# Kernel tuning notes

Hardware: AMD Instinct MI355X
Metric: run time of the kernel (lower is better)

The kernel has to match this reference:

```python
import jax, jax.numpy as jnp
import numpy as np

D_IN = 1024
D_OUT = 1024
NUM_HEADS = 16
HEAD_DIM = D_OUT // NUM_HEADS


def setup_inputs() -> dict:
    key = jax.random.key(0)
    k_x, k_q, k_k, k_v, k_o, k_ob = jax.random.split(key, 6)
    s_in = 1.0 / np.sqrt(D_IN)
    s_out = 1.0 / np.sqrt(D_OUT)
    return {
        "x": jax.random.normal(k_x, (4, 2048, D_IN), dtype=jnp.float32),
        "W_Q": jax.random.uniform(k_q, (D_IN, D_OUT), jnp.float32, -s_in, s_in),
        "W_K": jax.random.uniform(k_k, (D_IN, D_OUT), jnp.float32, -s_in, s_in),
        "W_V": jax.random.uniform(k_v, (D_IN, D_OUT), jnp.float32, -s_in, s_in),
        "W_O": jax.random.uniform(k_o, (D_OUT, D_OUT), jnp.float32, -s_out, s_out),
        "b_O": jax.random.uniform(k_ob, (D_OUT,), jnp.float32, -s_out, s_out),
    }


def reference(x, W_Q, W_K, W_V, W_O, b_O):
    B, T, _ = x.shape
    # projections -> [B, H, T, Dh]
    Q = (x @ W_Q).reshape(B, T, NUM_HEADS, HEAD_DIM).transpose(0, 2, 1, 3)
    K = (x @ W_K).reshape(B, T, NUM_HEADS, HEAD_DIM).transpose(0, 2, 1, 3)
    V = (x @ W_V).reshape(B, T, NUM_HEADS, HEAD_DIM).transpose(0, 2, 1, 3)
    scores = jnp.einsum("bhqd,bhkd->bhqk", Q, K) / np.sqrt(HEAD_DIM).astype(np.float32)
    causal = jnp.tril(jnp.ones((T, T), dtype=bool))  # True = keep
    scores = jnp.where(causal, scores, -jnp.inf)
    weights = jax.nn.softmax(scores, axis=-1)
    ctx = jnp.einsum("bhqk,bhkd->bhqd", weights, V)
    ctx = ctx.transpose(0, 2, 1, 3).reshape(B, T, D_OUT)
    return ctx @ W_O + b_O
```

## Files before the change

### kernel.cpp

```cpp
#include <hip/hip_runtime.h>

typedef unsigned short ushort_t;
typedef __attribute__((ext_vector_type(8))) __bf16 bf16x8;
typedef __attribute__((ext_vector_type(4))) float f32x4;
typedef __attribute__((ext_vector_type(16))) float f32x16;
typedef __attribute__((ext_vector_type(4))) unsigned short us4;
typedef __attribute__((ext_vector_type(8))) unsigned short us8;
typedef __attribute__((ext_vector_type(4))) unsigned int u32x4;

#define AS1 __attribute__((address_space(1)))
#define AS3 __attribute__((address_space(3)))

__device__ __forceinline__ unsigned short f2bf(float f) {
    unsigned u = __float_as_uint(f);
    u += 0x7fff + ((u >> 16) & 1);
    return (unsigned short)(u >> 16);
}

__device__ __forceinline__ unsigned cvtpk_bf16(float lo, float hi) {
    unsigned r;
    asm("v_cvt_pk_bf16_f32 %0, %1, %2" : "=v"(r) : "v"(lo), "v"(hi));
    return r;
}

__device__ __forceinline__ float fast_exp2(float x) {
    float r;
    asm("v_exp_f32 %0, %1" : "=v"(r) : "v"(x));
    return r;
}

__global__ void k_convert_x(const float* __restrict__ x, ushort_t* __restrict__ xb, int n4) {
    int i = blockIdx.x * blockDim.x + threadIdx.x;
    int stride = gridDim.x * blockDim.x;
    for (; i < n4; i += stride) {
        float4 f = reinterpret_cast<const float4*>(x)[i];
        us4 o = { f2bf(f.x), f2bf(f.y), f2bf(f.z), f2bf(f.w) };
        reinterpret_cast<us4*>(xb)[i] = o;
    }
}

__global__ void k_transpose_w(const float* __restrict__ wq, const float* __restrict__ wk,
                              const float* __restrict__ wv, const float* __restrict__ wo,
                              ushort_t* __restrict__ wqkvt, ushort_t* __restrict__ wot) {
    __shared__ float t[64][65];
    int bx = blockIdx.x;
    int w = bx >> 8;
    int ti = bx & 255;
    int k0 = (ti >> 4) * 64, n0 = (ti & 15) * 64;
    const float* src = (w == 0) ? wq : (w == 1) ? wk : (w == 2) ? wv : wo;
    ushort_t* dst = (w < 3) ? (wqkvt + (size_t)w * 1048576) : wot;
    for (int i = threadIdx.x; i < 4096; i += 256) {
        int r = i >> 6, c = i & 63;
        t[c][r] = src[(size_t)(k0 + r) * 1024 + n0 + c];
    }
    __syncthreads();
    for (int i = threadIdx.x; i < 4096; i += 256) {
        int r = i >> 6, c = i & 63;
        dst[(size_t)(n0 + r) * 1024 + k0 + c] = f2bf(t[r][c]);
    }
}

__global__ __launch_bounds__(512, 2) void k_gemm_qkv256(
    const ushort_t* __restrict__ A, const ushort_t* __restrict__ Bm,
    ushort_t* __restrict__ qd, ushort_t* __restrict__ kd, ushort_t* __restrict__ vd) {
    __shared__ __attribute__((aligned(16))) ushort_t lds[2 * 32768];

    const int tid = threadIdx.x, wid = tid >> 6, lane = tid & 63;
    const int lr = lane & 15, lg = lane >> 4;
    const int wm = wid >> 2, wn = wid & 3;

    int bid = blockIdx.x;
    int wg = (bid & 7) * 48 + (bid >> 3);
    const int by = wg / 12, bx = wg % 12;
    const int row0 = by * 256, col0 = bx * 256;

    const int srcrow = lane >> 2;
    const int srccol = (((lane & 3) * 16) ^ ((lane >> 5) << 5)) >> 1;
    const ushort_t* aS = A  + (size_t)(row0 + srcrow) * 1024 + srccol;
    const ushort_t* bS = Bm + (size_t)(col0 + srcrow) * 1024 + srccol;
    const int rdoff = (lr * 64 + lg * 16) ^ ((lr >> 3) << 5);

    const int s0 = (wid & 3) + ((wid >> 2) << 3);
    const int s1 = s0 + 4;

#define STG_A(kt, sr, sc) \
    __builtin_amdgcn_global_load_lds((const AS1 void*)(aS + (size_t)(sr) * 16384 + (kt) * 64 + (sc) * 32), \
        (AS3 void*)((AS3 char*)lds + (((kt) & 1) << 16) + (sr) * 2048 + (sc) * 1024), 16, 0, 0)
#define STG_B(kt, sr, sc) \
    __builtin_amdgcn_global_load_lds((const AS1 void*)(bS + (size_t)(sr) * 16384 + (kt) * 64 + (sc) * 32), \
        (AS3 void*)((AS3 char*)lds + (((kt) & 1) << 16) + 32768 + (sr) * 2048 + (sc) * 1024), 16, 0, 0)
#define ISSUE_P1(kt)  { STG_A(kt, s0, 0); }
#define ISSUE_P2(kt)  { STG_A(kt, s1, 0); STG_B(kt, 2 * wid, 0); STG_B(kt, 2 * wid + 1, 0); }
#define ISSUE_P3(kt)  { STG_A(kt, s0, 1); }
#define ISSUE_TOP(kt) { STG_A(kt, s1, 1); STG_B(kt, 2 * wid, 1); STG_B(kt, 2 * wid + 1, 1); }

    f32x4 acc[8][4] = {};

    ISSUE_P1(0); ISSUE_P2(0); ISSUE_P3(0); ISSUE_TOP(0);
    ISSUE_P1(1); ISSUE_P2(1); ISSUE_P3(1);

#pragma unroll 1
    for (int kt = 0; kt < 16; ++kt) {
        if (kt < 15) {
            ISSUE_TOP(kt + 1);
            asm volatile("s_waitcnt vmcnt(8)" ::: "memory");
        } else {
            asm volatile("s_waitcnt vmcnt(0)" ::: "memory");
        }
        __builtin_amdgcn_s_barrier();

        const char* bufA = (const char*)lds + ((kt & 1) << 16);
        const char* bufB = bufA + 32768;
        bf16x8 av[4], bv[4];

#pragma unroll
        for (int x = 0; x < 4; ++x) {
            av[x] = *reinterpret_cast<const bf16x8*>(bufA + (wm * 8 + x) * 2048 + rdoff);
            bv[x] = *reinterpret_cast<const bf16x8*>(bufB + (wn * 4 + x) * 2048 + rdoff);
        }
        __builtin_amdgcn_s_setprio(1);
#pragma unroll
        for (int mf = 0; mf < 4; ++mf)
#pragma unroll
            for (int nf = 0; nf < 4; ++nf)
                acc[mf][nf] = __builtin_amdgcn_mfma_f32_16x16x32_bf16(av[mf], bv[nf], acc[mf][nf], 0, 0, 0);
        __builtin_amdgcn_s_setprio(0);
        asm volatile("s_waitcnt lgkmcnt(0)" ::: "memory");
        __builtin_amdgcn_s_barrier();

        if (kt < 14) ISSUE_P1(kt + 2);
#pragma unroll
        for (int x = 0; x < 4; ++x)
            av[x] = *reinterpret_cast<const bf16x8*>(bufA + (wm * 8 + 4 + x) * 2048 + rdoff);
        __builtin_amdgcn_s_setprio(1);
#pragma unroll
        for (int mf = 0; mf < 4; ++mf)
#pragma unroll
            for (int nf = 0; nf < 4; ++nf)
                acc[4 + mf][nf] = __builtin_amdgcn_mfma_f32_16x16x32_bf16(av[mf], bv[nf], acc[4 + mf][nf], 0, 0, 0);
        __builtin_amdgcn_s_setprio(0);
        asm volatile("s_waitcnt lgkmcnt(0)" ::: "memory");
        __builtin_amdgcn_s_barrier();

        if (kt < 14) ISSUE_P2(kt + 2);
#pragma unroll
        for (int x = 0; x < 4; ++x) {
            av[x] = *reinterpret_cast<const bf16x8*>(bufA + (wm * 8 + x) * 2048 + 1024 + rdoff);
            bv[x] = *reinterpret_cast<const bf16x8*>(bufB + (wn * 4 + x) * 2048 + 1024 + rdoff);
        }
        __builtin_amdgcn_s_setprio(1);
#pragma unroll
        for (int mf = 0; mf < 4; ++mf)
#pragma unroll
            for (int nf = 0; nf < 4; ++nf)
                acc[mf][nf] = __builtin_amdgcn_mfma_f32_16x16x32_bf16(av[mf], bv[nf], acc[mf][nf], 0, 0, 0);
        __builtin_amdgcn_s_setprio(0);
        asm volatile("s_waitcnt lgkmcnt(0)" ::: "memory");
        __builtin_amdgcn_s_barrier();

        if (kt < 14) ISSUE_P3(kt + 2);
#pragma unroll
        for (int x = 0; x < 4; ++x)
            av[x] = *reinterpret_cast<const bf16x8*>(bufA + (wm * 8 + 4 + x) * 2048 + 1024 + rdoff);
        __builtin_amdgcn_s_setprio(1);
#pragma unroll
        for (int mf = 0; mf < 4; ++mf)
#pragma unroll
            for (int nf = 0; nf < 4; ++nf)
                acc[4 + mf][nf] = __builtin_amdgcn_mfma_f32_16x16x32_bf16(av[mf], bv[nf], acc[4 + mf][nf], 0, 0, 0);
        __builtin_amdgcn_s_setprio(0);
        asm volatile("s_waitcnt lgkmcnt(0)" ::: "memory");
        __builtin_amdgcn_s_barrier();
    }
#undef STG_A
#undef STG_B
#undef ISSUE_P1
#undef ISSUE_P2
#undef ISSUE_P3
#undef ISSUE_TOP

    const int w = bx >> 2;
    ushort_t* dst = (w == 0) ? qd : (w == 1) ? kd : vd;
    const float osc = (w == 0) ? 0.18033688f : 1.0f;
#pragma unroll
    for (int mi = 0; mi < 8; ++mi) {
#pragma unroll
        for (int nf = 0; nf < 4; ++nf) {
            int col = col0 + wn * 64 + nf * 16 + lr;
            int c1 = col & 1023;
            int h = c1 >> 6, dh = c1 & 63;
#pragma unroll
            for (int e = 0; e < 4; ++e) {
                int row = row0 + wm * 128 + mi * 16 + lg * 4 + e;
                int b = row >> 11, t = row & 2047;
                dst[(((size_t)(b * 16 + h)) * 2048 + t) * 64 + dh] = f2bf(acc[mi][nf][e] * osc);
            }
        }
    }
}

__global__ __launch_bounds__(256) void k_transpose_v(const ushort_t* __restrict__ vd,
                                                     ushort_t* __restrict__ vt) {
    __shared__ __attribute__((aligned(16))) ushort_t tile[64 * 72];
    int bid = blockIdx.x;
    int bh = bid >> 5, tt = bid & 31;
    const ushort_t* src = vd + ((size_t)bh * 2048 + tt * 64) * 64;
    ushort_t* dst = vt + (size_t)bh * 2048 * 64 + tt * 64;
#pragma unroll
    for (int r = 0; r < 2; ++r) {
        int i = r * 256 + threadIdx.x;
        int t = i >> 3, c8 = (i & 7) * 8;
        us8 v = *reinterpret_cast<const us8*>(src + (size_t)t * 64 + c8);
        *reinterpret_cast<us8*>(&tile[t * 72 + (c8 ^ ((t >> 3) << 3))]) = v;
    }
    __syncthreads();
#pragma unroll
    for (int r = 0; r < 2; ++r) {
        int i = r * 256 + threadIdx.x;
        int dh = i >> 3, t8 = (i & 7) * 8;
        us8 o;
#pragma unroll
        for (int e = 0; e < 8; ++e)
            o[e] = tile[(t8 + e) * 72 + (dh ^ ((t8 >> 3) << 3))];
        *reinterpret_cast<us8*>(dst + (size_t)dh * 2048 + t8) = o;
    }
}

__global__ __launch_bounds__(256) void k_attn(
    const ushort_t* __restrict__ q, const ushort_t* __restrict__ k,
    const ushort_t* __restrict__ v, ushort_t* __restrict__ ctx) {
    __shared__ __attribute__((aligned(16))) ushort_t lsK[2 * 8192];
    __shared__ __attribute__((aligned(16))) ushort_t lsV[2 * 8192];

    const int tid = threadIdx.x, wid = tid >> 6, lane = tid & 63;
    const int l31 = lane & 31, hi = lane >> 5;
    const int bid = blockIdx.x;
    const int bh = bid >> 3, pi = bid & 7;
    const size_t base = (size_t)bh * 2048 * 64;
    const ushort_t* qg = q + base;
    const ushort_t* kg = k + base;
    const ushort_t* vtg = v + base;
    const int b = bh >> 4, h = bh & 15;

    const int skey = wid * 8 + (lane >> 3);
    const int scb0 = ((lane & 7) * 16) ^ ((skey & 7) << 4);
    const int kx = (l31 & 7) << 4;
    int koffA[4];
#pragma unroll
    for (int s = 0; s < 4; ++s)
        koffA[s] = l31 * 128 + ((s * 32 + hi * 16) ^ kx);

    us8 ow;
#pragma unroll
    for (int e = 0; e < 8; ++e) ow[e] = 0x3F80;
    const bf16x8 onef = __builtin_bit_cast(bf16x8, ow);

#pragma unroll 1
    for (int pass = 0; pass < 2; ++pass) {
        const int qt = pass ? pi : (15 - pi);
        const int q0 = qt * 128;
        const int q0w = q0 + wid * 32;
        const int qrow = q0w + l31;
        const int njt = qt + 1;

        bf16x8 qf[4];
#pragma unroll
        for (int s = 0; s < 4; ++s)
            qf[s] = *reinterpret_cast<const bf16x8*>(qg + (size_t)qrow * 64 + s * 16 + hi * 8);

        const ushort_t* kpr[4];
        const ushort_t* vpr[4];
#pragma unroll
        for (int r = 0; r < 4; ++r) {
            kpr[r] = kg + (size_t)(r * 32 + skey) * 64 + (scb0 >> 1);
            vpr[r] = vtg + (size_t)((r & 1) * 32 + skey) * 2048 + (r >> 1) * 64 + (scb0 >> 1);
        }

        f32x16 acc0 = {}, acc1 = {}, lacc = {};

        __syncthreads();
#pragma unroll
        for (int r = 0; r < 4; ++r) {
            __builtin_amdgcn_global_load_lds((const AS1 void*)kpr[r],
                (AS3 void*)((AS3 char*)lsK + r * 4096 + wid * 1024), 16, 0, 0);
            __builtin_amdgcn_global_load_lds((const AS1 void*)vpr[r],
                (AS3 void*)((AS3 char*)lsV + r * 4096 + wid * 1024), 16, 0, 0);
        }

        unsigned bo = 0;
        for (int jt = 0; jt < njt; ++jt) {
            __syncthreads();
            const int j0 = jt << 7;
            if (jt + 1 < njt) {
                const unsigned nb = bo ^ 16384;
#pragma unroll
                for (int r = 0; r < 4; ++r) {
                    kpr[r] += 8192;
                    vpr[r] += 128;
                    __builtin_amdgcn_global_load_lds((const AS1 void*)kpr[r],
                        (AS3 void*)((AS3 char*)lsK + nb + r * 4096 + wid * 1024), 16, 0, 0);
                    __builtin_amdgcn_global_load_lds((const AS1 void*)vpr[r],
                        (AS3 void*)((AS3 char*)lsV + nb + r * 4096 + wid * 1024), 16, 0, 0);
                }
            }

#pragma unroll
            for (int hh = 0; hh < 2; ++hh) {
                const int j0h = j0 + hh * 64;
                if (j0h < q0w + 32) {
                    const char* bK = reinterpret_cast<const char*>(lsK) + bo + hh * 8192;
                    const char* bV = reinterpret_cast<const char*>(lsV) + bo + hh * 8192;

                    f32x16 s0 = {}, s1 = {};
#pragma unroll
                    for (int s = 0; s < 4; ++s) {
                        bf16x8 ka = *reinterpret_cast<const bf16x8*>(bK + koffA[s]);
                        s0 = __builtin_amdgcn_mfma_f32_32x32x16_bf16(ka, qf[s], s0, 0, 0, 0);
                    }
#pragma unroll
                    for (int s = 0; s < 4; ++s) {
                        bf16x8 ka = *reinterpret_cast<const bf16x8*>(bK + 4096 + koffA[s]);
                        s1 = __builtin_amdgcn_mfma_f32_32x32x16_bf16(ka, qf[s], s1, 0, 0, 0);
                    }

                    float p0[16], p1[16];
                    if (j0h + 63 > q0w) {
                        const int jh = j0h + 4 * hi;
#pragma unroll
                        for (int r = 0; r < 16; ++r) {
                            const int kl = jh + (r & 3) + 8 * (r >> 2);
                            float e0 = fast_exp2(s0[r]);
                            float e1 = fast_exp2(s1[r]);
                            p0[r] = (kl > qrow) ? 0.f : e0;
                            p1[r] = (kl + 32 > qrow) ? 0.f : e1;
                        }
                    } else {
#pragma unroll
                        for (int r = 0; r < 16; ++r) {
                            p0[r] = fast_exp2(s0[r]);
                            p1[r] = fast_exp2(s1[r]);
                        }
                    }

#pragma unroll
                    for (int kb = 0; kb < 2; ++kb) {
                        const float* pp = kb ? p1 : p0;
                        unsigned pw[8];
#pragma unroll
                        for (int g = 0; g < 4; ++g) {
                            pw[2 * g]     = cvtpk_bf16(pp[4 * g],     pp[4 * g + 1]);
                            pw[2 * g + 1] = cvtpk_bf16(pp[4 * g + 2], pp[4 * g + 3]);
                        }
#pragma unroll
                        for (int j = 0; j < 2; ++j) {
                            asm("v_permlane32_swap_b32 %0, %1" : "+v"(pw[4 * j]),     "+v"(pw[4 * j + 2]));
                            asm("v_permlane32_swap_b32 %0, %1" : "+v"(pw[4 * j + 1]), "+v"(pw[4 * j + 3]));
                            u32x4 fw = { pw[4 * j], pw[4 * j + 1], pw[4 * j + 2], pw[4 * j + 3] };
                            bf16x8 pf = __builtin_bit_cast(bf16x8, fw);
                            const int jj = kb * 2 + j;
                            {
                                bf16x8 vf = *reinterpret_cast<const bf16x8*>(bV + koffA[jj]);
                                acc0 = __builtin_amdgcn_mfma_f32_32x32x16_bf16(vf, pf, acc0, 0, 0, 0);
                            }
                            {
                                bf16x8 vf = *reinterpret_cast<const bf16x8*>(bV + 4096 + koffA[jj]);
                                acc1 = __builtin_amdgcn_mfma_f32_32x32x16_bf16(vf, pf, acc1, 0, 0, 0);
                            }
                            lacc = __builtin_amdgcn_mfma_f32_32x32x16_bf16(onef, pf, lacc, 0, 0, 0);
                        }
                    }
                }
            }
            bo ^= 16384;
        }

        float inv = 1.0f / lacc[0];
        size_t orow = ((size_t)(b * 2048 + qrow)) * 1024 + h * 64;
#pragma unroll
        for (int g = 0; g < 4; ++g) {
            us4 o0 = { f2bf(acc0[4 * g] * inv),     f2bf(acc0[4 * g + 1] * inv),
                       f2bf(acc0[4 * g + 2] * inv), f2bf(acc0[4 * g + 3] * inv) };
            *reinterpret_cast<us4*>(&ctx[orow + 8 * g + 4 * hi]) = o0;
            us4 o1 = { f2bf(acc1[4 * g] * inv),     f2bf(acc1[4 * g + 1] * inv),
                       f2bf(acc1[4 * g + 2] * inv), f2bf(acc1[4 * g + 3] * inv) };
            *reinterpret_cast<us4*>(&ctx[orow + 32 + 8 * g + 4 * hi]) = o1;
        }
    }
}

__global__ __launch_bounds__(256) void k_gemm_out(
    const ushort_t* __restrict__ cb, const ushort_t* __restrict__ wot,
    const float* __restrict__ bO, float* __restrict__ out) {
    __shared__ ushort_t lA[128 * 32];
    __shared__ ushort_t lB[128 * 32];
    const int tid = threadIdx.x, wid = tid >> 6, lane = tid & 63;
    const int lr = lane & 15, lg = lane >> 4;
    const int wm = wid >> 1, wn = wid & 1;
    const int bx = blockIdx.x;
    const int by = blockIdx.y;
    const int row0 = by * 128, col0 = bx * 128;
    const int crow = lane >> 2;
    const int coff = (lane & 3) * 8;

    f32x4 acc[4][4] = {};

    for (int k0 = 0; k0 < 1024; k0 += 32) {
        for (int c = wid; c < 8; c += 4) {
            const ushort_t* ga = cb + (size_t)(row0 + c * 16 + crow) * 1024 + k0 + coff;
            __builtin_amdgcn_global_load_lds((const AS1 void*)ga, (AS3 void*)(lA + c * 512), 16, 0, 0);
            const ushort_t* gb = wot + (size_t)(col0 + c * 16 + crow) * 1024 + k0 + coff;
            __builtin_amdgcn_global_load_lds((const AS1 void*)gb, (AS3 void*)(lB + c * 512), 16, 0, 0);
        }
        __syncthreads();
        bf16x8 af[4], bfr[4];
#pragma unroll
        for (int i = 0; i < 4; ++i) {
            af[i]  = *reinterpret_cast<const bf16x8*>(lA + (wm * 64 + i * 16 + lr) * 32 + lg * 8);
            bfr[i] = *reinterpret_cast<const bf16x8*>(lB + (wn * 64 + i * 16 + lr) * 32 + lg * 8);
        }
#pragma unroll
        for (int mi = 0; mi < 4; ++mi)
#pragma unroll
            for (int ni = 0; ni < 4; ++ni)
                acc[mi][ni] = __builtin_amdgcn_mfma_f32_16x16x32_bf16(af[mi], bfr[ni], acc[mi][ni], 0, 0, 0);
        __syncthreads();
    }

#pragma unroll
    for (int mi = 0; mi < 4; ++mi) {
#pragma unroll
        for (int ni = 0; ni < 4; ++ni) {
            int col = col0 + wn * 64 + ni * 16 + lr;
            float bias = bO[col];
#pragma unroll
            for (int e = 0; e < 4; ++e) {
                int row = row0 + wm * 64 + mi * 16 + lg * 4 + e;
                out[(size_t)row * 1024 + col] = acc[mi][ni][e] + bias;
            }
        }
    }
}

extern "C" void kernel_launch(void* const* d_in, const int* in_sizes, int n_in,
                              void* d_out, int out_size, void* d_ws, size_t ws_size,
                              hipStream_t stream) {
    const float* x  = (const float*)d_in[0];
    const float* wq = (const float*)d_in[1];
    const float* wk = (const float*)d_in[2];
    const float* wv = (const float*)d_in[3];
    const float* wo = (const float*)d_in[4];
    const float* bo = (const float*)d_in[5];
    float* out = (float*)d_out;

    char* ws = (char*)d_ws;
    ushort_t* xb    = (ushort_t*)(ws);
    ushort_t* wqkvt = (ushort_t*)(ws + 16777216);
    ushort_t* wot   = (ushort_t*)(ws + 23068672);
    ushort_t* qd    = (ushort_t*)(ws + 25165824);
    ushort_t* kd    = (ushort_t*)(ws + 41943040);
    ushort_t* vd    = (ushort_t*)(ws + 58720256);
    ushort_t* cd    = (ushort_t*)(ws + 75497472);
    ushort_t* vt    = xb;

    k_convert_x<<<2048, 256, 0, stream>>>(x, xb, 8192 * 1024 / 4);
    k_transpose_w<<<1024, 256, 0, stream>>>(wq, wk, wv, wo, wqkvt, wot);
    k_gemm_qkv256<<<384, 512, 0, stream>>>(xb, wqkvt, qd, kd, vd);
    k_transpose_v<<<2048, 256, 0, stream>>>(vd, vt);
    k_attn<<<512, 256, 0, stream>>>(qd, kd, vt, cd);
    k_gemm_out<<<dim3(8, 64), 256, 0, stream>>>(cd, wot, bo, out);
}
```

Before: 175.1 us.

## Retile QKV GEMM to 256x192 blocks with 512 workgroups and reworked load pipeline

The fused QKV projection GEMM moves from 256x256 tiles (384 workgroups) to 256x192 tiles (512 workgroups), so the grid divides evenly across the 256 CUs at two blocks per CU and avoids a partial second wave. The global-to-LDS staging groups and waitcnt schedule are reorganised: loads are issued after barriers, fragments are double-buffered in registers (av0/av1, bv0/bv1), and the explicit lgkmcnt waits and one barrier per phase are dropped. Tiles can now straddle the Q/K/V boundary, so output destination and scale are chosen per column. Each tile does less MFMA work per byte of A loaded, and the looser sync may expose LDS hazards or lower reuse.

```diff
diff --git a/kernel.cpp b/kernel.cpp
--- a/kernel.cpp
+++ b/kernel.cpp
@@ -63,16 +63,16 @@
 __global__ __launch_bounds__(512, 2) void k_gemm_qkv256(
     const ushort_t* __restrict__ A, const ushort_t* __restrict__ Bm,
     ushort_t* __restrict__ qd, ushort_t* __restrict__ kd, ushort_t* __restrict__ vd) {
-    __shared__ __attribute__((aligned(16))) ushort_t lds[2 * 32768];
+    __shared__ __attribute__((aligned(16))) ushort_t lds[2 * 28672];
 
     const int tid = threadIdx.x, wid = tid >> 6, lane = tid & 63;
     const int lr = lane & 15, lg = lane >> 4;
     const int wm = wid >> 2, wn = wid & 3;
 
     int bid = blockIdx.x;
-    int wg = (bid & 7) * 48 + (bid >> 3);
-    const int by = wg / 12, bx = wg % 12;
-    const int row0 = by * 256, col0 = bx * 256;
+    int wg = (bid & 7) * 64 + (bid >> 3);
+    const int by = wg >> 4, bx = wg & 15;
+    const int row0 = by * 256, col0 = bx * 192;
 
     const int srcrow = lane >> 2;
     const int srccol = (((lane & 3) * 16) ^ ((lane >> 5) << 5)) >> 1;
@@ -82,113 +82,110 @@
 
     const int s0 = (wid & 3) + ((wid >> 2) << 3);
     const int s1 = s0 + 4;
+    const int bmix_sr = 8 + (wid & 3);
+    const int bmix_sc = wid >> 2;
 
 #define STG_A(kt, sr, sc) \
     __builtin_amdgcn_global_load_lds((const AS1 void*)(aS + (size_t)(sr) * 16384 + (kt) * 64 + (sc) * 32), \
-        (AS3 void*)((AS3 char*)lds + (((kt) & 1) << 16) + (sr) * 2048 + (sc) * 1024), 16, 0, 0)
+        (AS3 void*)((AS3 char*)lds + ((kt) & 1) * 57344 + (sr) * 2048 + (sc) * 1024), 16, 0, 0)
 #define STG_B(kt, sr, sc) \
     __builtin_amdgcn_global_load_lds((const AS1 void*)(bS + (size_t)(sr) * 16384 + (kt) * 64 + (sc) * 32), \
-        (AS3 void*)((AS3 char*)lds + (((kt) & 1) << 16) + 32768 + (sr) * 2048 + (sc) * 1024), 16, 0, 0)
-#define ISSUE_P1(kt)  { STG_A(kt, s0, 0); }
-#define ISSUE_P2(kt)  { STG_A(kt, s1, 0); STG_B(kt, 2 * wid, 0); STG_B(kt, 2 * wid + 1, 0); }
-#define ISSUE_P3(kt)  { STG_A(kt, s0, 1); }
-#define ISSUE_TOP(kt) { STG_A(kt, s1, 1); STG_B(kt, 2 * wid, 1); STG_B(kt, 2 * wid + 1, 1); }
-
-    f32x4 acc[8][4] = {};
-
-    ISSUE_P1(0); ISSUE_P2(0); ISSUE_P3(0); ISSUE_TOP(0);
-    ISSUE_P1(1); ISSUE_P2(1); ISSUE_P3(1);
+        (AS3 void*)((AS3 char*)lds + ((kt) & 1) * 57344 + 32768 + (sr) * 2048 + (sc) * 1024), 16, 0, 0)
+#define GRP1(kt)  { STG_A(kt, s0, 0); STG_B(kt, wid, 0); }
+#define GRP2(kt)  { STG_A(kt, s1, 0); }
+#define GRP3(kt)  { STG_A(kt, s0, 1); STG_B(kt, wid, 1); }
+#define GTOP(kt)  { STG_A(kt, s1, 1); STG_B(kt, bmix_sr, bmix_sc); }
+
+    f32x4 acc[8][3] = {};
+
+    GRP1(0); GRP2(0); GRP3(0); GTOP(0);
+    GRP1(1); GRP2(1); GRP3(1);
 
 #pragma unroll 1
     for (int kt = 0; kt < 16; ++kt) {
-        if (kt < 15) {
-            ISSUE_TOP(kt + 1);
-            asm volatile("s_waitcnt vmcnt(8)" ::: "memory");
-        } else {
-            asm volatile("s_waitcnt vmcnt(0)" ::: "memory");
-        }
+        if (kt < 15) asm volatile("s_waitcnt vmcnt(5)" ::: "memory");
+        else         asm volatile("s_waitcnt vmcnt(0)" ::: "memory");
         __builtin_amdgcn_s_barrier();
-
-        const char* bufA = (const char*)lds + ((kt & 1) << 16);
+        if (kt < 15) GTOP(kt + 1);
+
+        const char* bufA = (const char*)lds + (kt & 1) * 57344;
         const char* bufB = bufA + 32768;
-        bf16x8 av[4], bv[4];
-
-#pragma unroll
-        for (int x = 0; x < 4; ++x) {
-            av[x] = *reinterpret_cast<const bf16x8*>(bufA + (wm * 8 + x) * 2048 + rdoff);
-            bv[x] = *reinterpret_cast<const bf16x8*>(bufB + (wn * 4 + x) * 2048 + rdoff);
-        }
+
+        bf16x8 av0[4], av1[4], bv0[3], bv1[3];
+#pragma unroll
+        for (int x = 0; x < 4; ++x)
+            av0[x] = *reinterpret_cast<const bf16x8*>(bufA + (wm * 8 + x) * 2048 + rdoff);
+#pragma unroll
+        for (int x = 0; x < 3; ++x)
+            bv0[x] = *reinterpret_cast<const bf16x8*>(bufB + (wn * 3 + x) * 2048 + rdoff);
+
+#pragma unroll
+        for (int x = 0; x < 4; ++x)
+            av1[x] = *reinterpret_cast<const bf16x8*>(bufA + (wm * 8 + 4 + x) * 2048 + rdoff);
         __builtin_amdgcn_s_setprio(1);
 #pragma unroll
         for (int mf = 0; mf < 4; ++mf)
 #pragma unroll
-            for (int nf = 0; nf < 4; ++nf)
-                acc[mf][nf] = __builtin_amdgcn_mfma_f32_16x16x32_bf16(av[mf], bv[nf], acc[mf][nf], 0, 0, 0);
+            for (int nf = 0; nf < 3; ++nf)
+                acc[mf][nf] = __builtin_amdgcn_mfma_f32_16x16x32_bf16(av0[mf], bv0[nf], acc[mf][nf], 0, 0, 0);
         __builtin_amdgcn_s_setprio(0);
-        asm volatile("s_waitcnt lgkmcnt(0)" ::: "memory");
         __builtin_amdgcn_s_barrier();
 
-        if (kt < 14) ISSUE_P1(kt + 2);
 #pragma unroll
         for (int x = 0; x < 4; ++x)
-            av[x] = *reinterpret_cast<const bf16x8*>(bufA + (wm * 8 + 4 + x) * 2048 + rdoff);
+            av0[x] = *reinterpret_cast<const bf16x8*>(bufA + (wm * 8 + x) * 2048 + 1024 + rdoff);
+#pragma unroll
+        for (int x = 0; x < 3; ++x)
+            bv1[x] = *reinterpret_cast<const bf16x8*>(bufB + (wn * 3 + x) * 2048 + 1024 + rdoff);
         __builtin_amdgcn_s_setprio(1);
 #pragma unroll
         for (int mf = 0; mf < 4; ++mf)
 #pragma unroll
-            for (int nf = 0; nf < 4; ++nf)
-                acc[4 + mf][nf] = __builtin_amdgcn_mfma_f32_16x16x32_bf16(av[mf], bv[nf], acc[4 + mf][nf], 0, 0, 0);
+            for (int nf = 0; nf < 3; ++nf)
+                acc[4 + mf][nf] = __builtin_amdgcn_mfma_f32_16x16x32_bf16(av1[mf], bv0[nf], acc[4 + mf][nf], 0, 0, 0);
         __builtin_amdgcn_s_setprio(0);
-        asm volatile("s_waitcnt lgkmcnt(0)" ::: "memory");
+        if (kt < 14) GRP1(kt + 2);
         __builtin_amdgcn_s_barrier();
 
-        if (kt < 14) ISSUE_P2(kt + 2);
-#pragma unroll
-        for (int x = 0; x < 4; ++x) {
-            av[x] = *reinterpret_cast<const bf16x8*>(bufA + (wm * 8 + x) * 2048 + 1024 + rdoff);
-            bv[x] = *reinterpret_cast<const bf16x8*>(bufB + (wn * 4 + x) * 2048 + 1024 + rdoff);
-        }
+#pragma unroll
+        for (int x = 0; x < 4; ++x)
+            av1[x] = *reinterpret_cast<const bf16x8*>(bufA + (wm * 8 + 4 + x) * 2048 + 1024 + rdoff);
         __builtin_amdgcn_s_setprio(1);
 #pragma unroll
         for (int mf = 0; mf < 4; ++mf)
 #pragma unroll
-            for (int nf = 0; nf < 4; ++nf)
-                acc[mf][nf] = __builtin_amdgcn_mfma_f32_16x16x32_bf16(av[mf], bv[nf], acc[mf][nf], 0, 0, 0);
+            for (int nf = 0; nf < 3; ++nf)
+                acc[mf][nf] = __builtin_amdgcn_mfma_f32_16x16x32_bf16(av0[mf], bv1[nf], acc[mf][nf], 0, 0, 0);
         __builtin_amdgcn_s_setprio(0);
-        asm volatile("s_waitcnt lgkmcnt(0)" ::: "memory");
+        if (kt < 14) GRP2(kt + 2);
         __builtin_amdgcn_s_barrier();
 
-        if (kt < 14) ISSUE_P3(kt + 2);
-#pragma unroll
-        for (int x = 0; x < 4; ++x)
-            av[x] = *reinterpret_cast<const bf16x8*>(bufA + (wm * 8 + 4 + x) * 2048 + 1024 + rdoff);
         __builtin_amdgcn_s_setprio(1);
 #pragma unroll
         for (int mf = 0; mf < 4; ++mf)
 #pragma unroll
-            for (int nf = 0; nf < 4; ++nf)
-                acc[4 + mf][nf] = __builtin_amdgcn_mfma_f32_16x16x32_bf16(av[mf], bv[nf], acc[4 + mf][nf], 0, 0, 0);
+            for (int nf = 0; nf < 3; ++nf)
+                acc[4 + mf][nf] = __builtin_amdgcn_mfma_f32_16x16x32_bf16(av1[mf], bv1[nf], acc[4 + mf][nf], 0, 0, 0);
         __builtin_amdgcn_s_setprio(0);
-        asm volatile("s_waitcnt lgkmcnt(0)" ::: "memory");
-        __builtin_amdgcn_s_barrier();
+        if (kt < 14) GRP3(kt + 2);
     }
 #undef STG_A
 #undef STG_B
-#undef ISSUE_P1
-#undef ISSUE_P2
-#undef ISSUE_P3
-#undef ISSUE_TOP
-
-    const int w = bx >> 2;
-    ushort_t* dst = (w == 0) ? qd : (w == 1) ? kd : vd;
-    const float osc = (w == 0) ? 0.18033688f : 1.0f;
+#undef GRP1
+#undef GRP2
+#undef GRP3
+#undef GTOP
+
 #pragma unroll
     for (int mi = 0; mi < 8; ++mi) {
 #pragma unroll
-        for (int nf = 0; nf < 4; ++nf) {
-            int col = col0 + wn * 64 + nf * 16 + lr;
+        for (int nf = 0; nf < 3; ++nf) {
+            int col = col0 + wn * 48 + nf * 16 + lr;
+            int w = col >> 10;
             int c1 = col & 1023;
             int h = c1 >> 6, dh = c1 & 63;
+            ushort_t* dst = (w == 0) ? qd : (w == 1) ? kd : vd;
+            const float osc = (w == 0) ? 0.18033688f : 1.0f;
 #pragma unroll
             for (int e = 0; e < 4; ++e) {
                 int row = row0 + wm * 128 + mi * 16 + lg * 4 + e;
@@ -464,7 +461,7 @@
 
     k_convert_x<<<2048, 256, 0, stream>>>(x, xb, 8192 * 1024 / 4);
     k_transpose_w<<<1024, 256, 0, stream>>>(wq, wk, wv, wo, wqkvt, wot);
-    k_gemm_qkv256<<<384, 512, 0, stream>>>(xb, wqkvt, qd, kd, vd);
+    k_gemm_qkv256<<<512, 512, 0, stream>>>(xb, wqkvt, qd, kd, vd);
     k_transpose_v<<<2048, 256, 0, stream>>>(vd, vt);
     k_attn<<<512, 256, 0, stream>>>(qd, kd, vt, cd);
     k_gemm_out<<<dim3(8, 64), 256, 0, stream>>>(cd, wot, bo, out);
```

Result: faster. 168.7 us (-3.7%).
